# Kernel tuning notes

Hardware: AMD Instinct MI355X
Metric: run time of the kernel (lower is better)

The kernel has to match this reference:

```python
import jax, jax.numpy as jnp
import numpy as np

DIM = 64; NFEATS = 32; DEPTH = 4; HEADS = 8; DIM_HEAD = 64
INNER = HEADS * DIM_HEAD            # 512
DI_COL = int(DIM * 4.0)             # 256
D_ROW = DIM * NFEATS                # 2048
DI_ROW = int(D_ROW * 0.5)           # 1024
B = 2048; NCAT = 16; NCONT = 16
EPS = 1e-5


def setup_inputs() -> dict:
    key = jax.random.key(0)
    ks = iter(jax.random.split(key, 32))
    def w(shape):
        return jax.random.normal(next(ks), shape, jnp.float32) * 0.02
    inp = {
        'x': jax.random.normal(next(ks), (B, NCAT, DIM), jnp.float32),
        'x_cont': jax.random.normal(next(ks), (B, NCONT, DIM), jnp.float32),
        # col-attention blocks (stacked over depth)
        'c_ln1_g': jnp.ones((DEPTH, DIM), jnp.float32),
        'c_ln1_b': jnp.zeros((DEPTH, DIM), jnp.float32),
        'c_wqkv': w((DEPTH, DIM, 3 * INNER)),
        'c_wo_w': w((DEPTH, INNER, DIM)),
        'c_wo_b': jnp.zeros((DEPTH, DIM), jnp.float32),
        'c_ln2_g': jnp.ones((DEPTH, DIM), jnp.float32),
        'c_ln2_b': jnp.zeros((DEPTH, DIM), jnp.float32),
        'c_w1': w((DEPTH, DIM, 2 * DI_COL)),
        'c_b1': jnp.zeros((DEPTH, 2 * DI_COL), jnp.float32),
        'c_w2': w((DEPTH, DI_COL, DIM)),
        'c_b2': jnp.zeros((DEPTH, DIM), jnp.float32),
        # row (intersample) blocks
        'r_ln1_g': jnp.ones((DEPTH, D_ROW), jnp.float32),
        'r_ln1_b': jnp.zeros((DEPTH, D_ROW), jnp.float32),
        'r_wqkv': w((DEPTH, D_ROW, 3 * INNER)),
        'r_wo_w': w((DEPTH, INNER, D_ROW)),
        'r_wo_b': jnp.zeros((DEPTH, D_ROW), jnp.float32),
        'r_ln2_g': jnp.ones((DEPTH, D_ROW), jnp.float32),
        'r_ln2_b': jnp.zeros((DEPTH, D_ROW), jnp.float32),
        'r_w1': w((DEPTH, D_ROW, 2 * DI_ROW)),
        'r_b1': jnp.zeros((DEPTH, 2 * DI_ROW), jnp.float32),
        'r_w2': w((DEPTH, DI_ROW, D_ROW)),
        'r_b2': jnp.zeros((DEPTH, D_ROW), jnp.float32),
    }
    return inp


def _ln(x, g, b):
    m = x.mean(-1, keepdims=True)
    v = ((x - m) ** 2).mean(-1, keepdims=True)
    return (x - m) / jnp.sqrt(v + EPS) * g + b


def _attn(x, wqkv, wo_w, wo_b):
    b, n, _ = x.shape
    q, k, v = jnp.split(x @ wqkv, 3, axis=-1)
    sp = lambda t: t.reshape(b, n, HEADS, DIM_HEAD).transpose(0, 2, 1, 3)
    q, k, v = sp(q), sp(k), sp(v)
    logits = jnp.einsum('bhid,bhjd->bhij', q, k) * (DIM_HEAD ** -0.5)
    a = jax.nn.softmax(logits, axis=-1)
    o = jnp.einsum('bhij,bhjd->bhid', a, v)
    o = o.transpose(0, 2, 1, 3).reshape(b, n, INNER)
    return o @ wo_w + wo_b


def _geglu_mlp(x, w1, b1, w2, b2):
    h = x @ w1 + b1
    a, g = jnp.split(h, 2, axis=-1)
    return (a * jax.nn.gelu(g, approximate=False)) @ w2 + b2


def _block(x, ln1g, ln1b, wqkv, wow, wob, ln2g, ln2b, w1, b1, w2, b2):
    # PreNorm(Residual(fn)): out = fn(LN(x)) + LN(x)  (residual on normalized x)
    xn = _ln(x, ln1g, ln1b)
    x = _attn(xn, wqkv, wow, wob) + xn
    xn = _ln(x, ln2g, ln2b)
    return _geglu_mlp(xn, w1, b1, w2, b2) + xn


def reference(x, x_cont,
              c_ln1_g, c_ln1_b, c_wqkv, c_wo_w, c_wo_b, c_ln2_g, c_ln2_b, c_w1, c_b1, c_w2, c_b2,
              r_ln1_g, r_ln1_b, r_wqkv, r_wo_w, r_wo_b, r_ln2_g, r_ln2_b, r_w1, r_b1, r_w2, r_b2):
    x = jnp.concatenate([x, x_cont], axis=1)  # [B, NFEATS, DIM]
    for i in range(DEPTH):
        # col: attention over features within each sample
        x = _block(x, c_ln1_g[i], c_ln1_b[i], c_wqkv[i], c_wo_w[i], c_wo_b[i],
                   c_ln2_g[i], c_ln2_b[i], c_w1[i], c_b1[i], c_w2[i], c_b2[i])
        # row: intersample attention, 'b n d -> 1 b (n d)'
        xr = x.reshape(1, B, D_ROW)
        xr = _block(xr, r_ln1_g[i], r_ln1_b[i], r_wqkv[i], r_wo_w[i], r_wo_b[i],
                    r_ln2_g[i], r_ln2_b[i], r_w1[i], r_b1[i], r_w2[i], r_b2[i])
        x = xr.reshape(B, NFEATS, DIM)
    return x
```

## Files before the change

kernel.cpp:

```cpp
#include <hip/hip_runtime.h>
#include <hip/hip_bf16.h>
#include <cstddef>

#define BD    2048
#define NF    32
#define DIMC  64
#define HEADS 8
#define DROW  2048
#define LNEPS 1e-5f

typedef __hip_bfloat16 bf16;
typedef __attribute__((ext_vector_type(8))) short short8;
typedef __attribute__((ext_vector_type(4))) float f32x4;

#define MFMA16 __builtin_amdgcn_mfma_f32_16x16x32_bf16

__device__ inline float ldin(const void* p, size_t i, int bf) {
    if (bf) return __bfloat162float(((const bf16*)p)[i]);
    return ((const float*)p)[i];
}

__device__ inline float gelu_exact(float x) {
    return 0.5f * x * (1.0f + erff(x * 0.70710678118654752f));
}

__global__ __launch_bounds__(64) void k_detect(const void* __restrict__ x,
                                               int* __restrict__ flag) {
    int i = threadIdx.x;
    size_t idx = (size_t)(2 * i) * 16384;
    unsigned short u = ((const unsigned short*)x)[idx];
    int e = (u >> 7) & 0xFF;
    int plausible = (e == 0) || (e >= 96 && e <= 132);
    unsigned long long m = __ballot(plausible);
    if (i == 0) *flag = (__popcll(m) >= 48) ? 1 : 0;
}

__global__ __launch_bounds__(256) void k_concat(const void* __restrict__ x,
                                                const void* __restrict__ xc,
                                                float* __restrict__ X,
                                                const int* __restrict__ flag) {
    const int bf = *flag;
    int i = blockIdx.x * 256 + threadIdx.x;
    int d = i & 63;
    int f = (i >> 6) & 31;
    int b = i >> 11;
    float v = (f < 16) ? ldin(x,  ((size_t)b * 16 + f) * 64 + d, bf)
                       : ldin(xc, ((size_t)b * 16 + (f - 16)) * 64 + d, bf);
    X[i] = v;
}

__global__ __launch_bounds__(256) void k_ln64(const float* __restrict__ in,
                                              float* __restrict__ out,
                                              bf16* __restrict__ outh,
                                              const void* __restrict__ g,
                                              const void* __restrict__ b,
                                              size_t eoff,
                                              const int* __restrict__ flag) {
    const int bf = *flag;
    int row  = blockIdx.x * 4 + (threadIdx.x >> 6);
    int lane = threadIdx.x & 63;
    float v = in[(size_t)row * 64 + lane];
    float s = v;
    #pragma unroll
    for (int off = 32; off; off >>= 1) s += __shfl_xor(s, off);
    float mean = s * (1.0f / 64.0f);
    float dx = v - mean;
    float s2 = dx * dx;
    #pragma unroll
    for (int off = 32; off; off >>= 1) s2 += __shfl_xor(s2, off);
    float inv = rsqrtf(s2 * (1.0f / 64.0f) + LNEPS);
    float o = dx * inv * ldin(g, eoff + lane, bf) + ldin(b, eoff + lane, bf);
    out[(size_t)row * 64 + lane]  = o;
    outh[(size_t)row * 64 + lane] = __float2bfloat16(o);
}

__global__ __launch_bounds__(256) void k_ln_row(const float* __restrict__ in,
                                                float* __restrict__ out,
                                                bf16* __restrict__ outh,
                                                const void* __restrict__ g,
                                                const void* __restrict__ b,
                                                size_t eoff,
                                                const int* __restrict__ flag) {
    const int bf = *flag;
    const int row = blockIdx.x, tid = threadIdx.x;
    __shared__ float red[4];
    const float* r = in + (size_t)row * DROW;
    float v[8];
    float s = 0.f;
    #pragma unroll
    for (int i = 0; i < 8; ++i) { v[i] = r[tid + i * 256]; s += v[i]; }
    #pragma unroll
    for (int off = 32; off; off >>= 1) s += __shfl_xor(s, off);
    if ((tid & 63) == 0) red[tid >> 6] = s;
    __syncthreads();
    float mean = (red[0] + red[1] + red[2] + red[3]) * (1.0f / DROW);
    __syncthreads();
    float s2 = 0.f;
    #pragma unroll
    for (int i = 0; i < 8; ++i) { float dx = v[i] - mean; s2 += dx * dx; }
    #pragma unroll
    for (int off = 32; off; off >>= 1) s2 += __shfl_xor(s2, off);
    if ((tid & 63) == 0) red[tid >> 6] = s2;
    __syncthreads();
    float inv = rsqrtf((red[0] + red[1] + red[2] + red[3]) * (1.0f / DROW) + LNEPS);
    #pragma unroll
    for (int i = 0; i < 8; ++i) {
        int j = tid + i * 256;
        float o = (v[i] - mean) * inv * ldin(g, eoff + j, bf) + ldin(b, eoff + j, bf);
        out[(size_t)row * DROW + j]  = o;
        outh[(size_t)row * DROW + j] = __float2bfloat16(o);
    }
}

__global__ __launch_bounds__(256) void k_castT(const void* __restrict__ in, size_t eoff,
                                               int R, int C,
                                               bf16* __restrict__ out,
                                               const int* __restrict__ flag) {
    const int bf = *flag;
    __shared__ bf16 tile[32][33];
    const int tx = threadIdx.x & 31, ty = threadIdx.x >> 5;
    const int bx = blockIdx.x, by = blockIdx.y;
    #pragma unroll
    for (int k = 0; k < 4; ++k) {
        int r = bx * 32 + ty + k * 8;
        int c = by * 32 + tx;
        tile[ty + k * 8][tx] = __float2bfloat16(ldin(in, eoff + (size_t)r * C + c, bf));
    }
    __syncthreads();
    #pragma unroll
    for (int k = 0; k < 4; ++k) {
        int oc = by * 32 + ty + k * 8;
        int orr = bx * 32 + tx;
        out[(size_t)oc * R + orr] = tile[tx][ty + k * 8];
    }
}

__global__ __launch_bounds__(256) void k_transpose_bf(const bf16* __restrict__ in, int ld,
                                                      int R, int C,
                                                      bf16* __restrict__ out) {
    __shared__ bf16 tile[32][33];
    const int tx = threadIdx.x & 31, ty = threadIdx.x >> 5;
    const int bx = blockIdx.x, by = blockIdx.y;
    #pragma unroll
    for (int k = 0; k < 4; ++k) {
        int r = bx * 32 + ty + k * 8;
        int c = by * 32 + tx;
        tile[ty + k * 8][tx] = in[(size_t)r * ld + c];
    }
    __syncthreads();
    #pragma unroll
    for (int k = 0; k < 4; ++k) {
        int oc = by * 32 + ty + k * 8;
        int orr = bx * 32 + tx;
        out[(size_t)oc * R + orr] = tile[tx][ty + k * 8];
    }
}

template <int WM, int WN>
__global__ __launch_bounds__(256) void k_mfma_sk(
    int M, int N, int KC,
    const bf16* __restrict__ A, int lda,
    const bf16* __restrict__ Bt, int ldb,
    float* __restrict__ Cp, long long pstride)
{
    constexpr int TM = WM * 64, TN = WN * 64;
    const int z = blockIdx.z;
    const int m0 = blockIdx.y * TM, n0 = blockIdx.x * TN;
    const int tid = threadIdx.x, lane = tid & 63, wave = tid >> 6;
    const int wy = wave / WN, wx = wave % WN;
    __shared__ short As[TM][72];
    __shared__ short Bs[TN][72];
    f32x4 acc[4][4] = {};
    const int row8 = tid >> 3, chunk = (tid & 7) * 8;
    const int kend = z * KC + KC;
    for (int k0 = z * KC; k0 < kend; k0 += 64) {
        #pragma unroll
        for (int i = 0; i < TM / 32; ++i) {
            int r = i * 32 + row8;
            *(short8*)&As[r][chunk] =
                *(const short8*)(A + (size_t)(m0 + r) * lda + k0 + chunk);
        }
        #pragma unroll
        for (int i = 0; i < TN / 32; ++i) {
            int r = i * 32 + row8;
            *(short8*)&Bs[r][chunk] =
                *(const short8*)(Bt + (size_t)(n0 + r) * ldb + k0 + chunk);
        }
        __syncthreads();
        #pragma unroll
        for (int ks = 0; ks < 64; ks += 32) {
            short8 af[4], bfr[4];
            #pragma unroll
            for (int mt = 0; mt < 4; ++mt)
                af[mt] = *(const short8*)&As[wy * 64 + mt * 16 + (lane & 15)][ks + (lane >> 4) * 8];
            #pragma unroll
            for (int nt = 0; nt < 4; ++nt)
                bfr[nt] = *(const short8*)&Bs[wx * 64 + nt * 16 + (lane & 15)][ks + (lane >> 4) * 8];
            #pragma unroll
            for (int mt = 0; mt < 4; ++mt)
                #pragma unroll
                for (int nt = 0; nt < 4; ++nt)
                    acc[mt][nt] = MFMA16(af[mt], bfr[nt], acc[mt][nt], 0, 0, 0);
        }
        __syncthreads();
    }
    float* Co = Cp + (size_t)z * pstride;
    #pragma unroll
    for (int mt = 0; mt < 4; ++mt)
        #pragma unroll
        for (int r = 0; r < 4; ++r) {
            int m = m0 + wy * 64 + mt * 16 + (lane >> 4) * 4 + r;
            #pragma unroll
            for (int nt = 0; nt < 4; ++nt) {
                int n = n0 + wx * 64 + nt * 16 + (lane & 15);
                Co[(size_t)m * N + n] = acc[mt][nt][r];
            }
        }
}

template <bool OBF>
__global__ __launch_bounds__(256) void k_combine(
    int KS, const float* __restrict__ P, long long pstride, int N,
    void* __restrict__ C,
    const void* __restrict__ bias, size_t biasOff,
    const float* __restrict__ addend,
    const int* __restrict__ flag)
{
    int i = blockIdx.x * 256 + threadIdx.x;
    float v = 0.f;
    for (int z = 0; z < KS; ++z) v += P[(size_t)z * pstride + i];
    if (bias)   v += ldin(bias, biasOff + (size_t)(i % N), bias ? *flag : 0);
    if (addend) v += addend[i];
    if constexpr (OBF) ((bf16*)C)[i] = __float2bfloat16(v);
    else               ((float*)C)[i] = v;
}

__device__ inline void proj_tile(const short8 xa[2][2], const bf16* __restrict__ wbase,
                                 int l15, int quad, f32x4 c[2][4]) {
    #pragma unroll
    for (int nt = 0; nt < 4; ++nt) {
        short8 b0 = *(const short8*)(wbase + (size_t)(nt * 16 + l15) * 64 + quad * 8);
        short8 b1 = *(const short8*)(wbase + (size_t)(nt * 16 + l15) * 64 + 32 + quad * 8);
        #pragma unroll
        for (int mt = 0; mt < 2; ++mt) {
            c[mt][nt] = MFMA16(xa[mt][0], b0, c[mt][nt], 0, 0, 0);
            c[mt][nt] = MFMA16(xa[mt][1], b1, c[mt][nt], 0, 0, 0);
        }
    }
}

__global__ __launch_bounds__(256) void k_col_qkv_attn(
    const bf16* __restrict__ Xh, const bf16* __restrict__ Wt,
    bf16* __restrict__ Oh)
{
    __shared__ __align__(16) short bufA[4][2304];
    __shared__ __align__(16) short bufB[4][2304];
    const int tid = threadIdx.x, lane = tid & 63, wave = tid >> 6;
    const int task = blockIdx.x * 4 + wave;
    const int s = task >> 3, h = task & 7;
    const int l15 = lane & 15, quad = lane >> 4;
    short* A  = bufA[wave];
    short* Bb = bufB[wave];

    short8 xa[2][2];
    #pragma unroll
    for (int mt = 0; mt < 2; ++mt)
        #pragma unroll
        for (int kc = 0; kc < 2; ++kc)
            xa[mt][kc] = *(const short8*)(Xh + (size_t)(s * 32 + mt * 16 + l15) * 64 + kc * 32 + quad * 8);

    {
        f32x4 c[2][4] = {};
        proj_tile(xa, Wt + (size_t)(h * 64) * 64, l15, quad, c);
        #pragma unroll
        for (int mt = 0; mt < 2; ++mt)
            #pragma unroll
            for (int nt = 0; nt < 4; ++nt)
                #pragma unroll
                for (int r = 0; r < 4; ++r)
                    *(bf16*)&A[(mt * 16 + quad * 4 + r) * 72 + nt * 16 + l15] =
                        __float2bfloat16(c[mt][nt][r]);
    }
    {
        f32x4 c[2][4] = {};
        proj_tile(xa, Wt + (size_t)(512 + h * 64) * 64, l15, quad, c);
        #pragma unroll
        for (int mt = 0; mt < 2; ++mt)
            #pragma unroll
            for (int nt = 0; nt < 4; ++nt)
                #pragma unroll
                for (int r = 0; r < 4; ++r)
                    *(bf16*)&Bb[(mt * 16 + quad * 4 + r) * 72 + nt * 16 + l15] =
                        __float2bfloat16(c[mt][nt][r]);
    }
    f32x4 S[2][2] = {};
    #pragma unroll
    for (int mt = 0; mt < 2; ++mt) {
        short8 qa0 = *(const short8*)&A[(mt * 16 + l15) * 72 + quad * 8];
        short8 qa1 = *(const short8*)&A[(mt * 16 + l15) * 72 + 32 + quad * 8];
        #pragma unroll
        for (int nt = 0; nt < 2; ++nt) {
            short8 kb0 = *(const short8*)&Bb[(nt * 16 + l15) * 72 + quad * 8];
            short8 kb1 = *(const short8*)&Bb[(nt * 16 + l15) * 72 + 32 + quad * 8];
            S[mt][nt] = MFMA16(qa0, kb0, S[mt][nt], 0, 0, 0);
            S[mt][nt] = MFMA16(qa1, kb1, S[mt][nt], 0, 0, 0);
        }
    }
    {
        f32x4 c[2][4] = {};
        proj_tile(xa, Wt + (size_t)(1024 + h * 64) * 64, l15, quad, c);
        #pragma unroll
        for (int mt = 0; mt < 2; ++mt)
            #pragma unroll
            for (int nt = 0; nt < 4; ++nt)
                #pragma unroll
                for (int r = 0; r < 4; ++r)
                    *(bf16*)&Bb[(nt * 16 + l15) * 36 + mt * 16 + quad * 4 + r] =
                        __float2bfloat16(c[mt][nt][r]);
    }
    float inv[2][4];
    #pragma unroll
    for (int mt = 0; mt < 2; ++mt) {
        #pragma unroll
        for (int ri = 0; ri < 4; ++ri) {
            float e0 = __expf(S[mt][0][ri] * 0.125f);
            float e1 = __expf(S[mt][1][ri] * 0.125f);
            float sum = e0 + e1;
            #pragma unroll
            for (int msk = 1; msk < 16; msk <<= 1) sum += __shfl_xor(sum, msk);
            inv[mt][ri] = 1.0f / sum;
            int row = mt * 16 + quad * 4 + ri;
            *(bf16*)&A[row * 72 + l15]      = __float2bfloat16(e0);
            *(bf16*)&A[row * 72 + 16 + l15] = __float2bfloat16(e1);
        }
    }
    short8 pa[2];
    #pragma unroll
    for (int mt = 0; mt < 2; ++mt)
        pa[mt] = *(const short8*)&A[(mt * 16 + l15) * 72 + quad * 8];
    f32x4 O[2][4] = {};
    #pragma unroll
    for (int nt = 0; nt < 4; ++nt) {
        short8 vb = *(const short8*)&Bb[(nt * 16 + l15) * 36 + quad * 8];
        #pragma unroll
        for (int mt = 0; mt < 2; ++mt)
            O[mt][nt] = MFMA16(pa[mt], vb, O[mt][nt], 0, 0, 0);
    }
    #pragma unroll
    for (int mt = 0; mt < 2; ++mt)
        #pragma unroll
        for (int nt = 0; nt < 4; ++nt)
            #pragma unroll
            for (int ri = 0; ri < 4; ++ri) {
                size_t row = (size_t)s * 32 + mt * 16 + quad * 4 + ri;
                Oh[row * 512 + h * 64 + nt * 16 + l15] =
                    __float2bfloat16(O[mt][nt][ri] * inv[mt][ri]);
            }
}

__global__ __launch_bounds__(256) void k_col_wo(
    const bf16* __restrict__ Oh, const bf16* __restrict__ Wt,
    const void* __restrict__ bias, size_t biasOff,
    const float* __restrict__ XN, float* __restrict__ ACC,
    const int* __restrict__ flag)
{
    const int lane = threadIdx.x & 63, wave = threadIdx.x >> 6;
    const int rb = (blockIdx.x * 4 + wave) * 32;
    const int l15 = lane & 15, quad = lane >> 4;
    f32x4 acc[2][4] = {};
    #pragma unroll 2
    for (int kc = 0; kc < 512; kc += 32) {
        short8 a0 = *(const short8*)(Oh + (size_t)(rb + l15) * 512 + kc + quad * 8);
        short8 a1 = *(const short8*)(Oh + (size_t)(rb + 16 + l15) * 512 + kc + quad * 8);
        #pragma unroll
        for (int nt = 0; nt < 4; ++nt) {
            short8 b = *(const short8*)(Wt + (size_t)(nt * 16 + l15) * 512 + kc + quad * 8);
            acc[0][nt] = MFMA16(a0, b, acc[0][nt], 0, 0, 0);
            acc[1][nt] = MFMA16(a1, b, acc[1][nt], 0, 0, 0);
        }
    }
    const int bf = *flag;
    #pragma unroll
    for (int nt = 0; nt < 4; ++nt) {
        float bv = ldin(bias, biasOff + nt * 16 + l15, bf);
        #pragma unroll
        for (int mt = 0; mt < 2; ++mt)
            #pragma unroll
            for (int r = 0; r < 4; ++r) {
                size_t idx = (size_t)(rb + mt * 16 + quad * 4 + r) * 64 + nt * 16 + l15;
                ACC[idx] = acc[mt][nt][r] + bv + XN[idx];
            }
    }
}

__global__ __launch_bounds__(256) void k_col_mlp(
    const bf16* __restrict__ Xh,
    const bf16* __restrict__ W1t,
    const bf16* __restrict__ W2t,
    const void* __restrict__ b1, size_t b1Off,
    const void* __restrict__ b2, size_t b2Off,
    const float* __restrict__ XN, float* __restrict__ Xout,
    const int* __restrict__ flag)
{
    __shared__ __align__(16) short Pl[4][32][72];
    const int lane = threadIdx.x & 63, wave = threadIdx.x >> 6;
    const int rb = (blockIdx.x * 4 + wave) * 32;
    const int l15 = lane & 15, quad = lane >> 4;
    const int bf = *flag;
    short (*P)[72] = Pl[wave];

    short8 xa[2][2];
    #pragma unroll
    for (int mt = 0; mt < 2; ++mt)
        #pragma unroll
        for (int kc = 0; kc < 2; ++kc)
            xa[mt][kc] = *(const short8*)(Xh + (size_t)(rb + mt * 16 + l15) * 64 + kc * 32 + quad * 8);

    f32x4 xacc[2][4] = {};
    #pragma unroll
    for (int jc = 0; jc < 256; jc += 64) {
        f32x4 ca[2][4] = {}, cg[2][4] = {};
        #pragma unroll
        for (int nt = 0; nt < 4; ++nt) {
            const bf16* wa = W1t + (size_t)(jc + nt * 16 + l15) * 64;
            short8 a0 = *(const short8*)(wa + quad * 8);
            short8 a1 = *(const short8*)(wa + 32 + quad * 8);
            const bf16* wg = W1t + (size_t)(256 + jc + nt * 16 + l15) * 64;
            short8 g0 = *(const short8*)(wg + quad * 8);
            short8 g1 = *(const short8*)(wg + 32 + quad * 8);
            #pragma unroll
            for (int mt = 0; mt < 2; ++mt) {
                ca[mt][nt] = MFMA16(xa[mt][0], a0, ca[mt][nt], 0, 0, 0);
                ca[mt][nt] = MFMA16(xa[mt][1], a1, ca[mt][nt], 0, 0, 0);
                cg[mt][nt] = MFMA16(xa[mt][0], g0, cg[mt][nt], 0, 0, 0);
                cg[mt][nt] = MFMA16(xa[mt][1], g1, cg[mt][nt], 0, 0, 0);
            }
        }
        #pragma unroll
        for (int nt = 0; nt < 4; ++nt) {
            float ba = ldin(b1, b1Off + jc + nt * 16 + l15, bf);
            float bg = ldin(b1, b1Off + 256 + jc + nt * 16 + l15, bf);
            #pragma unroll
            for (int mt = 0; mt < 2; ++mt)
                #pragma unroll
                for (int r = 0; r < 4; ++r) {
                    float p = (ca[mt][nt][r] + ba) * gelu_exact(cg[mt][nt][r] + bg);
                    *(bf16*)&P[mt * 16 + quad * 4 + r][nt * 16 + l15] = __float2bfloat16(p);
                }
        }
        short8 p0[2], p1[2];
        #pragma unroll
        for (int mt = 0; mt < 2; ++mt) {
            p0[mt] = *(const short8*)&P[mt * 16 + l15][quad * 8];
            p1[mt] = *(const short8*)&P[mt * 16 + l15][32 + quad * 8];
        }
        #pragma unroll
        for (int nt = 0; nt < 4; ++nt) {
            short8 w0 = *(const short8*)(W2t + (size_t)(nt * 16 + l15) * 256 + jc + quad * 8);
            short8 w1 = *(const short8*)(W2t + (size_t)(nt * 16 + l15) * 256 + jc + 32 + quad * 8);
            #pragma unroll
            for (int mt = 0; mt < 2; ++mt) {
                xacc[mt][nt] = MFMA16(p0[mt], w0, xacc[mt][nt], 0, 0, 0);
                xacc[mt][nt] = MFMA16(p1[mt], w1, xacc[mt][nt], 0, 0, 0);
            }
        }
    }
    #pragma unroll
    for (int nt = 0; nt < 4; ++nt) {
        float bv = ldin(b2, b2Off + nt * 16 + l15, bf);
        #pragma unroll
        for (int mt = 0; mt < 2; ++mt)
            #pragma unroll
            for (int r = 0; r < 4; ++r) {
                size_t idx = (size_t)(rb + mt * 16 + quad * 4 + r) * 64 + nt * 16 + l15;
                Xout[idx] = xacc[mt][nt][r] + bv + XN[idx];
            }
    }
}

__global__ __launch_bounds__(256) void k_flash_row(
    const bf16* __restrict__ QKV, const bf16* __restrict__ Vt,
    float* __restrict__ Opart, float* __restrict__ ML)
{
    __shared__ __align__(16) short Ps[4][16][136];
    const int tid = threadIdx.x, lane = tid & 63, wave = tid >> 6;
    const int h = blockIdx.y, z = blockIdx.z;
    const int q0 = blockIdx.x * 64 + wave * 16;
    const int l15 = lane & 15, quad = lane >> 4;

    short8 qa[2];
    #pragma unroll
    for (int kc = 0; kc < 2; ++kc)
        qa[kc] = *(const short8*)(QKV + (size_t)(q0 + l15) * 1536 + h * 64 + kc * 32 + quad * 8);

    float mi[4], li[4];
    #pragma unroll
    for (int r = 0; r < 4; ++r) { mi[r] = -1e30f; li[r] = 0.f; }
    f32x4 Oa[4] = {};

    #pragma unroll
    for (int jj = 0; jj < 4; ++jj) {
        const int j = z * 4 + jj;
        f32x4 s[8] = {};
        #pragma unroll
        for (int nt = 0; nt < 8; ++nt) {
            const bf16* krow = QKV + (size_t)(j * 128 + nt * 16 + l15) * 1536 + 512 + h * 64;
            short8 kb0 = *(const short8*)(krow + quad * 8);
            short8 kb1 = *(const short8*)(krow + 32 + quad * 8);
            s[nt] = MFMA16(qa[0], kb0, s[nt], 0, 0, 0);
            s[nt] = MFMA16(qa[1], kb1, s[nt], 0, 0, 0);
        }
        #pragma unroll
        for (int r = 0; r < 4; ++r) {
            float mt = -1e30f;
            #pragma unroll
            for (int nt = 0; nt < 8; ++nt) { s[nt][r] *= 0.125f; mt = fmaxf(mt, s[nt][r]); }
            #pragma unroll
            for (int msk = 1; msk < 16; msk <<= 1) mt = fmaxf(mt, __shfl_xor(mt, msk));
            float mn = fmaxf(mi[r], mt);
            float alpha = __expf(mi[r] - mn);
            float ls = 0.f;
            #pragma unroll
            for (int nt = 0; nt < 8; ++nt) { float p = __expf(s[nt][r] - mn); s[nt][r] = p; ls += p; }
            #pragma unroll
            for (int msk = 1; msk < 16; msk <<= 1) ls += __shfl_xor(ls, msk);
            li[r] = li[r] * alpha + ls;
            mi[r] = mn;
            #pragma unroll
            for (int nt = 0; nt < 4; ++nt) Oa[nt][r] *= alpha;
            int row = quad * 4 + r;
            #pragma unroll
            for (int nt = 0; nt < 8; ++nt)
                *(bf16*)&Ps[wave][row][nt * 16 + l15] = __float2bfloat16(s[nt][r]);
        }
        short8 pa[4];
        #pragma unroll
        for (int kc = 0; kc < 4; ++kc)
            pa[kc] = *(const short8*)&Ps[wave][l15][kc * 32 + quad * 8];
        #pragma unroll
        for (int nt = 0; nt < 4; ++nt) {
            #pragma unroll
            for (int kc = 0; kc < 4; ++kc) {
                short8 vb = *(const short8*)(Vt + (size_t)(h * 64 + nt * 16 + l15) * 2048 +
                                             j * 128 + kc * 32 + quad * 8);
                Oa[nt] = MFMA16(pa[kc], vb, Oa[nt], 0, 0, 0);
            }
        }
    }
    float* Op = Opart + (size_t)z * 1048576;
    #pragma unroll
    for (int nt = 0; nt < 4; ++nt)
        #pragma unroll
        for (int r = 0; r < 4; ++r)
            Op[(size_t)(q0 + quad * 4 + r) * 512 + h * 64 + nt * 16 + l15] = Oa[nt][r];
    if (l15 == 0) {
        #pragma unroll
        for (int r = 0; r < 4; ++r) {
            int row = q0 + quad * 4 + r;
            ML[((size_t)(z * 8 + h) * 2048 + row) * 2]     = mi[r];
            ML[((size_t)(z * 8 + h) * 2048 + row) * 2 + 1] = li[r];
        }
    }
}

__global__ __launch_bounds__(256) void k_flash_combine(
    const float* __restrict__ Opart, const float* __restrict__ ML,
    bf16* __restrict__ O)
{
    int i = blockIdx.x * 256 + threadIdx.x;
    int row = i >> 9, n = i & 511, h = n >> 6;
    float m[4], l[4], M = -1e30f;
    #pragma unroll
    for (int z = 0; z < 4; ++z) {
        m[z] = ML[((size_t)(z * 8 + h) * 2048 + row) * 2];
        l[z] = ML[((size_t)(z * 8 + h) * 2048 + row) * 2 + 1];
        M = fmaxf(M, m[z]);
    }
    float num = 0.f, den = 0.f;
    #pragma unroll
    for (int z = 0; z < 4; ++z) {
        float w = __expf(m[z] - M);
        num += w * Opart[(size_t)z * 1048576 + i];
        den += w * l[z];
    }
    O[i] = __float2bfloat16(num / den);
}

__global__ __launch_bounds__(256) void k_geglu_row(const float* __restrict__ H,
                                                   bf16* __restrict__ P) {
    int i = blockIdx.x * 256 + threadIdx.x;
    int r = i >> 10, j = i & 1023;
    float a = H[(size_t)r * 2048 + j];
    float g = H[(size_t)r * 2048 + 1024 + j];
    P[i] = __float2bfloat16(a * gelu_exact(g));
}

__global__ __launch_bounds__(256) void k_cast_out(const float* __restrict__ X,
                                                  void* __restrict__ out,
                                                  const int* __restrict__ flag) {
    const int bf = *flag;
    int i = blockIdx.x * 256 + threadIdx.x;
    if (bf) ((bf16*)out)[i] = __float2bfloat16(X[i]);
    else    ((float*)out)[i] = X[i];
}

extern "C" void kernel_launch(void* const* d_in, const int* in_sizes, int n_in,
                              void* d_out, int out_size, void* d_ws, size_t ws_size,
                              hipStream_t stream) {
    const void* x       = d_in[0];
    const void* x_cont  = d_in[1];
    const void* c_ln1_g = d_in[2];
    const void* c_ln1_b = d_in[3];
    const void* c_wqkv  = d_in[4];
    const void* c_wo_w  = d_in[5];
    const void* c_wo_b  = d_in[6];
    const void* c_ln2_g = d_in[7];
    const void* c_ln2_b = d_in[8];
    const void* c_w1    = d_in[9];
    const void* c_b1    = d_in[10];
    const void* c_w2    = d_in[11];
    const void* c_b2    = d_in[12];
    const void* r_ln1_g = d_in[13];
    const void* r_ln1_b = d_in[14];
    const void* r_wqkv  = d_in[15];
    const void* r_wo_w  = d_in[16];
    const void* r_wo_b  = d_in[17];
    const void* r_ln2_g = d_in[18];
    const void* r_ln2_b = d_in[19];
    const void* r_w1    = d_in[20];
    const void* r_b1    = d_in[21];
    const void* r_w2    = d_in[22];
    const void* r_b2    = d_in[23];

    const size_t NX = (size_t)BD * NF * DIMC;
    float* X   = (float*)d_ws;
    float* XN  = X   + NX;
    float* ACC = XN  + NX;
    bf16* XNh  = (bf16*)(ACC + NX);
    bf16* WtR  = XNh + NX;
    bf16* WcQ  = WtR + (size_t)2048 * 2048;
    bf16* WcO  = WcQ + 98304;
    bf16* Wc1  = WcO + 32768;
    bf16* Wc2  = Wc1 + 32768;
    bf16* Sc   = Wc2 + 16384;

    bf16*  OhC  = Sc;
    bf16*  QKVhR = Sc;
    bf16*  VtR   = QKVhR + 3145728;
    bf16*  OhR   = VtR + 1048576;
    bf16*  PmR   = OhR + 1048576;
    float* Hrow  = (float*)(PmR + 2097152);
    float* GpR   = (float*)((char*)Sc + 33554432);
    float* MLp   = GpR + (size_t)4 * 1048576;

    char* scEnd = (char*)Sc + 100663296;
    int*  flag  = (int*)scEnd;
    const size_t need = (size_t)(scEnd + 64 - (char*)d_ws);
    if (ws_size < need) return;

    k_detect<<<1, 64, 0, stream>>>(x, flag);
    k_concat<<<16384, 256, 0, stream>>>(x, x_cont, X, flag);

    for (int d = 0; d < 4; ++d) {
        k_ln64<<<16384, 256, 0, stream>>>(X, XN, XNh, c_ln1_g, c_ln1_b, (size_t)d * 64, flag);
        k_castT<<<dim3(2, 48), 256, 0, stream>>>(c_wqkv, (size_t)d * 64 * 1536, 64, 1536, WcQ, flag);
        k_col_qkv_attn<<<4096, 256, 0, stream>>>(XNh, WcQ, OhC);
        k_castT<<<dim3(16, 2), 256, 0, stream>>>(c_wo_w, (size_t)d * 512 * 64, 512, 64, WcO, flag);
        k_col_wo<<<512, 256, 0, stream>>>(OhC, WcO, c_wo_b, (size_t)d * 64, XN, ACC, flag);
        k_ln64<<<16384, 256, 0, stream>>>(ACC, XN, XNh, c_ln2_g, c_ln2_b, (size_t)d * 64, flag);
        k_castT<<<dim3(2, 16), 256, 0, stream>>>(c_w1, (size_t)d * 64 * 512, 64, 512, Wc1, flag);
        k_castT<<<dim3(8, 2), 256, 0, stream>>>(c_w2, (size_t)d * 256 * 64, 256, 64, Wc2, flag);
        k_col_mlp<<<512, 256, 0, stream>>>(XNh, Wc1, Wc2,
                                           c_b1, (size_t)d * 512, c_b2, (size_t)d * 64,
                                           XN, X, flag);

        k_ln_row<<<BD, 256, 0, stream>>>(X, XN, XNh, r_ln1_g, r_ln1_b, (size_t)d * DROW, flag);
        k_castT<<<dim3(64, 48), 256, 0, stream>>>(r_wqkv, (size_t)d * 2048 * 1536, 2048, 1536, WtR, flag);
        k_mfma_sk<2, 2><<<dim3(12, 16, 4), 256, 0, stream>>>(
            2048, 1536, 512, XNh, 2048, WtR, 2048, GpR, 3145728);
        k_combine<true><<<12288, 256, 0, stream>>>(
            4, GpR, 3145728, 1536, QKVhR, nullptr, 0, nullptr, flag);
        k_transpose_bf<<<dim3(64, 16), 256, 0, stream>>>(QKVhR + 1024, 1536, 2048, 512, VtR);
        k_flash_row<<<dim3(32, 8, 4), 256, 0, stream>>>(QKVhR, VtR, GpR, MLp);
        k_flash_combine<<<4096, 256, 0, stream>>>(GpR, MLp, OhR);
        k_castT<<<dim3(16, 64), 256, 0, stream>>>(r_wo_w, (size_t)d * 512 * 2048, 512, 2048, WtR, flag);
        k_mfma_sk<2, 2><<<dim3(16, 16, 4), 256, 0, stream>>>(
            2048, 2048, 128, OhR, 512, WtR, 512, GpR, 4194304);
        k_combine<false><<<16384, 256, 0, stream>>>(
            4, GpR, 4194304, 2048, ACC, r_wo_b, (size_t)d * DROW, XN, flag);
        k_ln_row<<<BD, 256, 0, stream>>>(ACC, XN, XNh, r_ln2_g, r_ln2_b, (size_t)d * DROW, flag);
        k_castT<<<dim3(64, 64), 256, 0, stream>>>(r_w1, (size_t)d * 2048 * 2048, 2048, 2048, WtR, flag);
        k_mfma_sk<2, 2><<<dim3(16, 16, 4), 256, 0, stream>>>(
            2048, 2048, 512, XNh, 2048, WtR, 2048, GpR, 4194304);
        k_combine<false><<<16384, 256, 0, stream>>>(
            4, GpR, 4194304, 2048, Hrow, r_b1, (size_t)d * 2048, nullptr, flag);
        k_geglu_row<<<8192, 256, 0, stream>>>(Hrow, PmR);
        k_castT<<<dim3(32, 64), 256, 0, stream>>>(r_w2, (size_t)d * 1024 * 2048, 1024, 2048, WtR, flag);
        k_mfma_sk<2, 2><<<dim3(16, 16, 4), 256, 0, stream>>>(
            2048, 2048, 256, PmR, 1024, WtR, 1024, GpR, 4194304);
        k_combine<false><<<16384, 256, 0, stream>>>(
            4, GpR, 4194304, 2048, X, r_b2, (size_t)d * DROW, XN, flag);
    }

    k_cast_out<<<16384, 256, 0, stream>>>(X, d_out, flag);
}
```

Before: 2.107 ms.

## Fuse split-K combine with LayerNorm/GEGLU/cast and merge Wq·Wkᵀ in column attention

The split-K partial-sum reduction is folded into the following LayerNorm, GEGLU, and output-cast steps. This removes intermediate float buffers (ACC, Hrow) and several full-tensor passes. For column attention, the per-head Wq·Wkᵀ is precomputed as a 64x64 matrix with the softmax scale folded in. Logits then come from (X·M)·Xᵀ, which avoids a separate K projection and its shared-memory round trip, at the cost of extra bf16 rounding of the merged weight.

```diff
diff --git a/kernel.cpp b/kernel.cpp
--- a/kernel.cpp
+++ b/kernel.cpp
@@ -133,6 +133,14 @@
         int orr = bx * 32 + tx;
         out[(size_t)oc * R + orr] = tile[tx][ty + k * 8];
     }
+}
+
+__global__ __launch_bounds__(256) void k_cast_qkv(const void* __restrict__ in, size_t eoff,
+                                                  bf16* __restrict__ out,
+                                                  const int* __restrict__ flag) {
+    const int bf = *flag;
+    int i = blockIdx.x * 256 + threadIdx.x;
+    out[i] = __float2bfloat16(ldin(in, eoff + i, bf));
 }
 
 __global__ __launch_bounds__(256) void k_transpose_bf(const bf16* __restrict__ in, int ld,
@@ -235,6 +243,141 @@
     else               ((float*)C)[i] = v;
 }
 
+__global__ __launch_bounds__(256) void k_comb_ln_row(
+    const float* __restrict__ P, long long pstride,
+    const void* __restrict__ bias, size_t biasOff,
+    float* XN, bf16* __restrict__ XNh,
+    const void* __restrict__ g, const void* __restrict__ b, size_t eoff,
+    const int* __restrict__ flag)
+{
+    const int bf = *flag;
+    const int row = blockIdx.x, tid = threadIdx.x;
+    __shared__ float red[4];
+    float v[8];
+    float s = 0.f;
+    #pragma unroll
+    for (int i = 0; i < 8; ++i) {
+        int j = tid + i * 256;
+        size_t idx = (size_t)row * DROW + j;
+        float t = P[idx] + P[pstride + idx] + P[2 * pstride + idx] + P[3 * pstride + idx];
+        t += ldin(bias, biasOff + j, bf) + XN[idx];
+        v[i] = t; s += t;
+    }
+    #pragma unroll
+    for (int off = 32; off; off >>= 1) s += __shfl_xor(s, off);
+    if ((tid & 63) == 0) red[tid >> 6] = s;
+    __syncthreads();
+    float mean = (red[0] + red[1] + red[2] + red[3]) * (1.0f / DROW);
+    __syncthreads();
+    float s2 = 0.f;
+    #pragma unroll
+    for (int i = 0; i < 8; ++i) { float dx = v[i] - mean; s2 += dx * dx; }
+    #pragma unroll
+    for (int off = 32; off; off >>= 1) s2 += __shfl_xor(s2, off);
+    if ((tid & 63) == 0) red[tid >> 6] = s2;
+    __syncthreads();
+    float inv = rsqrtf((red[0] + red[1] + red[2] + red[3]) * (1.0f / DROW) + LNEPS);
+    #pragma unroll
+    for (int i = 0; i < 8; ++i) {
+        int j = tid + i * 256;
+        float o = (v[i] - mean) * inv * ldin(g, eoff + j, bf) + ldin(b, eoff + j, bf);
+        XN[(size_t)row * DROW + j]  = o;
+        XNh[(size_t)row * DROW + j] = __float2bfloat16(o);
+    }
+}
+
+__global__ __launch_bounds__(256) void k_comb_geglu(
+    const float* __restrict__ P, long long pstride,
+    const void* __restrict__ b1, size_t b1Off,
+    bf16* __restrict__ Out,
+    const int* __restrict__ flag)
+{
+    const int bf = *flag;
+    int i = blockIdx.x * 256 + threadIdx.x;
+    int r = i >> 10, j = i & 1023;
+    size_t ia = (size_t)r * 2048 + j, ig = ia + 1024;
+    float a = P[ia] + P[pstride + ia] + P[2 * pstride + ia] + P[3 * pstride + ia]
+            + ldin(b1, b1Off + j, bf);
+    float gv = P[ig] + P[pstride + ig] + P[2 * pstride + ig] + P[3 * pstride + ig]
+            + ldin(b1, b1Off + 1024 + j, bf);
+    Out[i] = __float2bfloat16(a * gelu_exact(gv));
+}
+
+__global__ __launch_bounds__(256) void k_comb_ln64(
+    const float* __restrict__ P, long long pstride,
+    const void* __restrict__ bias, size_t biasOff,
+    float* XN, bf16* __restrict__ XNh,
+    const void* __restrict__ g, const void* __restrict__ b, size_t eoff,
+    const int* __restrict__ flag)
+{
+    const int bf = *flag;
+    int row  = blockIdx.x * 4 + (threadIdx.x >> 6);
+    int lane = threadIdx.x & 63;
+    size_t idx = (size_t)row * 64 + lane;
+    float v = P[idx] + P[pstride + idx] + P[2 * pstride + idx] + P[3 * pstride + idx]
+            + ldin(bias, biasOff + (idx & 2047), bf) + XN[idx];
+    float s = v;
+    #pragma unroll
+    for (int off = 32; off; off >>= 1) s += __shfl_xor(s, off);
+    float mean = s * (1.0f / 64.0f);
+    float dx = v - mean;
+    float s2 = dx * dx;
+    #pragma unroll
+    for (int off = 32; off; off >>= 1) s2 += __shfl_xor(s2, off);
+    float inv = rsqrtf(s2 * (1.0f / 64.0f) + LNEPS);
+    float o = dx * inv * ldin(g, eoff + lane, bf) + ldin(b, eoff + lane, bf);
+    XN[idx]  = o;
+    XNh[idx] = __float2bfloat16(o);
+}
+
+__global__ __launch_bounds__(256) void k_comb_cast(
+    const float* __restrict__ P, long long pstride,
+    const void* __restrict__ bias, size_t biasOff,
+    const float* __restrict__ XN,
+    void* __restrict__ out,
+    const int* __restrict__ flag)
+{
+    const int bf = *flag;
+    int i = blockIdx.x * 256 + threadIdx.x;
+    float v = P[i] + P[(size_t)pstride + i] + P[2 * (size_t)pstride + i] + P[3 * (size_t)pstride + i]
+            + ldin(bias, biasOff + (size_t)(i & 2047), bf) + XN[i];
+    if (bf) ((bf16*)out)[i] = __float2bfloat16(v);
+    else    ((float*)out)[i] = v;
+}
+
+__global__ __launch_bounds__(256) void k_qk_merge(
+    const bf16* __restrict__ Wh,
+    bf16* __restrict__ Mt)
+{
+    const int lane = threadIdx.x & 63, wave = threadIdx.x >> 6;
+    const int h = blockIdx.x * 4 + wave;
+    const int l15 = lane & 15, quad = lane >> 4;
+    f32x4 acc[4][4] = {};
+    #pragma unroll
+    for (int kc = 0; kc < 2; ++kc) {
+        short8 af[4], bfr[4];
+        #pragma unroll
+        for (int mt = 0; mt < 4; ++mt)
+            af[mt] = *(const short8*)(Wh + (size_t)(mt * 16 + l15) * 1536 + h * 64 + kc * 32 + quad * 8);
+        #pragma unroll
+        for (int nt = 0; nt < 4; ++nt)
+            bfr[nt] = *(const short8*)(Wh + (size_t)(nt * 16 + l15) * 1536 + 512 + h * 64 + kc * 32 + quad * 8);
+        #pragma unroll
+        for (int mt = 0; mt < 4; ++mt)
+            #pragma unroll
+            for (int nt = 0; nt < 4; ++nt)
+                acc[mt][nt] = MFMA16(af[mt], bfr[nt], acc[mt][nt], 0, 0, 0);
+    }
+    #pragma unroll
+    for (int mt = 0; mt < 4; ++mt)
+        #pragma unroll
+        for (int nt = 0; nt < 4; ++nt)
+            #pragma unroll
+            for (int r = 0; r < 4; ++r)
+                Mt[(size_t)h * 4096 + (nt * 16 + l15) * 64 + mt * 16 + quad * 4 + r] =
+                    __float2bfloat16(acc[mt][nt][r] * 0.125f);
+}
+
 __device__ inline void proj_tile(const short8 xa[2][2], const bf16* __restrict__ wbase,
                                  int l15, int quad, f32x4 c[2][4]) {
     #pragma unroll
@@ -251,7 +394,7 @@
 
 __global__ __launch_bounds__(256) void k_col_qkv_attn(
     const bf16* __restrict__ Xh, const bf16* __restrict__ Wt,
-    bf16* __restrict__ Oh)
+    const bf16* __restrict__ Mt, bf16* __restrict__ Oh)
 {
     __shared__ __align__(16) short bufA[4][2304];
     __shared__ __align__(16) short bufB[4][2304];
@@ -271,7 +414,7 @@
 
     {
         f32x4 c[2][4] = {};
-        proj_tile(xa, Wt + (size_t)(h * 64) * 64, l15, quad, c);
+        proj_tile(xa, Mt + (size_t)h * 4096, l15, quad, c);
         #pragma unroll
         for (int mt = 0; mt < 2; ++mt)
             #pragma unroll
@@ -283,31 +426,6 @@
     }
     {
         f32x4 c[2][4] = {};
-        proj_tile(xa, Wt + (size_t)(512 + h * 64) * 64, l15, quad, c);
-        #pragma unroll
-        for (int mt = 0; mt < 2; ++mt)
-            #pragma unroll
-            for (int nt = 0; nt < 4; ++nt)
-                #pragma unroll
-                for (int r = 0; r < 4; ++r)
-                    *(bf16*)&Bb[(mt * 16 + quad * 4 + r) * 72 + nt * 16 + l15] =
-                        __float2bfloat16(c[mt][nt][r]);
-    }
-    f32x4 S[2][2] = {};
-    #pragma unroll
-    for (int mt = 0; mt < 2; ++mt) {
-        short8 qa0 = *(const short8*)&A[(mt * 16 + l15) * 72 + quad * 8];
-        short8 qa1 = *(const short8*)&A[(mt * 16 + l15) * 72 + 32 + quad * 8];
-        #pragma unroll
-        for (int nt = 0; nt < 2; ++nt) {
-            short8 kb0 = *(const short8*)&Bb[(nt * 16 + l15) * 72 + quad * 8];
-            short8 kb1 = *(const short8*)&Bb[(nt * 16 + l15) * 72 + 32 + quad * 8];
-            S[mt][nt] = MFMA16(qa0, kb0, S[mt][nt], 0, 0, 0);
-            S[mt][nt] = MFMA16(qa1, kb1, S[mt][nt], 0, 0, 0);
-        }
-    }
-    {
-        f32x4 c[2][4] = {};
         proj_tile(xa, Wt + (size_t)(1024 + h * 64) * 64, l15, quad, c);
         #pragma unroll
         for (int mt = 0; mt < 2; ++mt)
@@ -318,13 +436,24 @@
                     *(bf16*)&Bb[(nt * 16 + l15) * 36 + mt * 16 + quad * 4 + r] =
                         __float2bfloat16(c[mt][nt][r]);
     }
+    f32x4 S[2][2] = {};
+    #pragma unroll
+    for (int mt = 0; mt < 2; ++mt) {
+        short8 ta0 = *(const short8*)&A[(mt * 16 + l15) * 72 + quad * 8];
+        short8 ta1 = *(const short8*)&A[(mt * 16 + l15) * 72 + 32 + quad * 8];
+        #pragma unroll
+        for (int nt = 0; nt < 2; ++nt) {
+            S[mt][nt] = MFMA16(ta0, xa[nt][0], S[mt][nt], 0, 0, 0);
+            S[mt][nt] = MFMA16(ta1, xa[nt][1], S[mt][nt], 0, 0, 0);
+        }
+    }
     float inv[2][4];
     #pragma unroll
     for (int mt = 0; mt < 2; ++mt) {
         #pragma unroll
         for (int ri = 0; ri < 4; ++ri) {
-            float e0 = __expf(S[mt][0][ri] * 0.125f);
-            float e1 = __expf(S[mt][1][ri] * 0.125f);
+            float e0 = __expf(S[mt][0][ri]);
+            float e1 = __expf(S[mt][1][ri]);
             float sum = e0 + e1;
             #pragma unroll
             for (int msk = 1; msk < 16; msk <<= 1) sum += __shfl_xor(sum, msk);
@@ -584,24 +713,6 @@
         den += w * l[z];
     }
     O[i] = __float2bfloat16(num / den);
-}
-
-__global__ __launch_bounds__(256) void k_geglu_row(const float* __restrict__ H,
-                                                   bf16* __restrict__ P) {
-    int i = blockIdx.x * 256 + threadIdx.x;
-    int r = i >> 10, j = i & 1023;
-    float a = H[(size_t)r * 2048 + j];
-    float g = H[(size_t)r * 2048 + 1024 + j];
-    P[i] = __float2bfloat16(a * gelu_exact(g));
-}
-
-__global__ __launch_bounds__(256) void k_cast_out(const float* __restrict__ X,
-                                                  void* __restrict__ out,
-                                                  const int* __restrict__ flag) {
-    const int bf = *flag;
-    int i = blockIdx.x * 256 + threadIdx.x;
-    if (bf) ((bf16*)out)[i] = __float2bfloat16(X[i]);
-    else    ((float*)out)[i] = X[i];
 }
 
 extern "C" void kernel_launch(void* const* d_in, const int* in_sizes, int n_in,
@@ -642,14 +753,15 @@
     bf16* WcO  = WcQ + 98304;
     bf16* Wc1  = WcO + 32768;
     bf16* Wc2  = Wc1 + 32768;
-    bf16* Sc   = Wc2 + 16384;
+    bf16* McQ  = Wc2 + 16384;
+    bf16* WqkvH= McQ + 32768;
+    bf16* Sc   = WqkvH + 98304;
 
     bf16*  OhC  = Sc;
     bf16*  QKVhR = Sc;
     bf16*  VtR   = QKVhR + 3145728;
     bf16*  OhR   = VtR + 1048576;
     bf16*  PmR   = OhR + 1048576;
-    float* Hrow  = (float*)(PmR + 2097152);
     float* GpR   = (float*)((char*)Sc + 33554432);
     float* MLp   = GpR + (size_t)4 * 1048576;
 
@@ -660,11 +772,13 @@
 
     k_detect<<<1, 64, 0, stream>>>(x, flag);
     k_concat<<<16384, 256, 0, stream>>>(x, x_cont, X, flag);
+    k_ln64<<<16384, 256, 0, stream>>>(X, XN, XNh, c_ln1_g, c_ln1_b, 0, flag);
 
     for (int d = 0; d < 4; ++d) {
-        k_ln64<<<16384, 256, 0, stream>>>(X, XN, XNh, c_ln1_g, c_ln1_b, (size_t)d * 64, flag);
         k_castT<<<dim3(2, 48), 256, 0, stream>>>(c_wqkv, (size_t)d * 64 * 1536, 64, 1536, WcQ, flag);
-        k_col_qkv_attn<<<4096, 256, 0, stream>>>(XNh, WcQ, OhC);
+        k_cast_qkv<<<384, 256, 0, stream>>>(c_wqkv, (size_t)d * 64 * 1536, WqkvH, flag);
+        k_qk_merge<<<2, 256, 0, stream>>>(WqkvH, McQ);
+        k_col_qkv_attn<<<4096, 256, 0, stream>>>(XNh, WcQ, McQ, OhC);
         k_castT<<<dim3(16, 2), 256, 0, stream>>>(c_wo_w, (size_t)d * 512 * 64, 512, 64, WcO, flag);
         k_col_wo<<<512, 256, 0, stream>>>(OhC, WcO, c_wo_b, (size_t)d * 64, XN, ACC, flag);
         k_ln64<<<16384, 256, 0, stream>>>(ACC, XN, XNh, c_ln2_g, c_ln2_b, (size_t)d * 64, flag);
@@ -686,21 +800,22 @@
         k_castT<<<dim3(16, 64), 256, 0, stream>>>(r_wo_w, (size_t)d * 512 * 2048, 512, 2048, WtR, flag);
         k_mfma_sk<2, 2><<<dim3(16, 16, 4), 256, 0, stream>>>(
             2048, 2048, 128, OhR, 512, WtR, 512, GpR, 4194304);
-        k_combine<false><<<16384, 256, 0, stream>>>(
-            4, GpR, 4194304, 2048, ACC, r_wo_b, (size_t)d * DROW, XN, flag);
-        k_ln_row<<<BD, 256, 0, stream>>>(ACC, XN, XNh, r_ln2_g, r_ln2_b, (size_t)d * DROW, flag);
+        k_comb_ln_row<<<BD, 256, 0, stream>>>(
+            GpR, 4194304, r_wo_b, (size_t)d * DROW, XN, XNh,
+            r_ln2_g, r_ln2_b, (size_t)d * DROW, flag);
         k_castT<<<dim3(64, 64), 256, 0, stream>>>(r_w1, (size_t)d * 2048 * 2048, 2048, 2048, WtR, flag);
         k_mfma_sk<2, 2><<<dim3(16, 16, 4), 256, 0, stream>>>(
             2048, 2048, 512, XNh, 2048, WtR, 2048, GpR, 4194304);
-        k_combine<false><<<16384, 256, 0, stream>>>(
-            4, GpR, 4194304, 2048, Hrow, r_b1, (size_t)d * 2048, nullptr, flag);
-        k_geglu_row<<<8192, 256, 0, stream>>>(Hrow, PmR);
+        k_comb_geglu<<<8192, 256, 0, stream>>>(GpR, 4194304, r_b1, (size_t)d * 2048, PmR, flag);
         k_castT<<<dim3(32, 64), 256, 0, stream>>>(r_w2, (size_t)d * 1024 * 2048, 1024, 2048, WtR, flag);
         k_mfma_sk<2, 2><<<dim3(16, 16, 4), 256, 0, stream>>>(
             2048, 2048, 256, PmR, 1024, WtR, 1024, GpR, 4194304);
-        k_combine<false><<<16384, 256, 0, stream>>>(
-            4, GpR, 4194304, 2048, X, r_b2, (size_t)d * DROW, XN, flag);
-    }
-
-    k_cast_out<<<16384, 256, 0, stream>>>(X, d_out, flag);
-}
+        if (d < 3)
+            k_comb_ln64<<<16384, 256, 0, stream>>>(
+                GpR, 4194304, r_b2, (size_t)d * DROW, XN, XNh,
+                c_ln1_g, c_ln1_b, (size_t)(d + 1) * 64, flag);
+        else
+            k_comb_cast<<<16384, 256, 0, stream>>>(
+                GpR, 4194304, r_b2, (size_t)d * DROW, XN, d_out, flag);
+    }
+}
```

After: 1.924 ms. -8.7%, faster.
